# Optimization experiments

Measured on AMD Instinct MI355X. Metric: run time of the kernel, lower is better.

## Reference

```python
import jax, jax.numpy as jnp
import numpy as np

B, N, D = 8, 500, 256
H, W = 480, 640
NUM_CORNERS = 500
MATCH_RADIUS = 1.0
SCORE_RADIUS = 8
BETA = (1.0, 1.0, 1.0)


def _rodrigues(aa):
    theta = jnp.linalg.norm(aa, axis=-1, keepdims=True)
    k = aa / jnp.maximum(theta, 1e-8)
    kx, ky, kz = k[..., 0], k[..., 1], k[..., 2]
    z = jnp.zeros_like(kx)
    Km = jnp.stack([jnp.stack([z, -kz, ky], -1),
                    jnp.stack([kz, z, -kx], -1),
                    jnp.stack([-ky, kx, z], -1)], -2)
    th = theta[..., None]
    return jnp.eye(3) + jnp.sin(th) * Km + (1. - jnp.cos(th)) * (Km @ Km)


def setup_inputs() -> dict:
    key = jax.random.key(0)
    ks = jax.random.split(key, 8)
    descriptors = jax.random.normal(ks[0], (B, N, D), jnp.float32)
    points = jax.random.uniform(ks[1], (B, N, 2), jnp.float32, -1.0, 1.0)
    pointness = jax.random.uniform(ks[2], (B, 1, H, W), jnp.float32) * 0.98 + 0.01
    depths_dense = jax.random.uniform(ks[3], (B, 1, H, W), jnp.float32) * 4.0 + 1.0
    imgs = jax.random.uniform(ks[4], (B, 3, H, W), jnp.float32)
    aa = jax.random.normal(ks[5], (B, 3), jnp.float32) * 0.02
    t = jax.random.normal(ks[6], (B, 3), jnp.float32) * 0.05
    R = _rodrigues(aa)
    poses = jnp.tile(jnp.eye(4, dtype=jnp.float32), (B, 1, 1))
    poses = poses.at[:, :3, :3].set(R).at[:, :3, 3].set(t)
    Kmat = jnp.tile(jnp.array([[300., 0., W / 2.], [0., 300., H / 2.], [0., 0., 1.]], jnp.float32), (B, 1, 1))
    return {"descriptors": descriptors, "points": points, "pointness": pointness,
            "depths_dense": depths_dense, "poses": poses, "K": Kmat, "imgs": imgs}


def denormalize(pts, h, w):
    return jnp.stack([(pts[..., 0] + 1.) * 0.5 * (w - 1), (pts[..., 1] + 1.) * 0.5 * (h - 1)], -1)


def normalize_pix(pts, h, w):
    return jnp.stack([2. * pts[..., 0] / (w - 1) - 1., 2. * pts[..., 1] / (h - 1) - 1.], -1)


def bilinear_sample(img, px):  # img (H,W), px (...,2) pixel coords
    x = jnp.clip(px[..., 0], 0., W - 1.)
    y = jnp.clip(px[..., 1], 0., H - 1.)
    x0 = jnp.floor(x); y0 = jnp.floor(y)
    x1 = jnp.minimum(x0 + 1., W - 1.); y1 = jnp.minimum(y0 + 1., H - 1.)
    wx = x - x0; wy = y - y0
    x0i = x0.astype(jnp.int32); x1i = x1.astype(jnp.int32)
    y0i = y0.astype(jnp.int32); y1i = y1.astype(jnp.int32)
    v00 = img[y0i, x0i]; v01 = img[y0i, x1i]
    v10 = img[y1i, x0i]; v11 = img[y1i, x1i]
    return v00 * (1 - wx) * (1 - wy) + v01 * wx * (1 - wy) + v10 * (1 - wx) * wy + v11 * wx * wy


def pairwise_project(pts, depths, poses, Kmat):
    # pts (B,N,2) normalized; proj[i,j] = points of frame i projected into frame j
    px = denormalize(pts, H, W)
    d = jax.vmap(bilinear_sample)(depths[:, 0], px)  # (B,Np)
    Kinv = jnp.linalg.inv(Kmat)
    homog = jnp.concatenate([px, jnp.ones_like(px[..., :1])], -1)
    Xc = d[..., None] * jnp.einsum('bij,bnj->bni', Kinv, homog)
    Rm = poses[:, :3, :3]; t = poses[:, :3, 3]
    Xw = jnp.einsum('bij,bnj->bni', Rm, Xc) + t[:, None, :]
    diff = Xw[:, None, :, :] - t[None, :, None, :]           # (src,dst,Np,3)
    Xj = jnp.einsum('jba,ijnb->ijna', Rm, diff)              # R_j^T (Xw - t_j)
    uvw = jnp.einsum('jab,ijnb->ijna', Kmat, Xj)
    z = uvw[..., 2]
    zs = jnp.where(jnp.abs(z) < 1e-6, 1e-6, z)
    pn = normalize_pix(jnp.stack([uvw[..., 0] / zs, uvw[..., 1] / zs], -1), H, W)
    invis = (z <= 1e-6) | (jnp.abs(pn[..., 0]) > 1.) | (jnp.abs(pn[..., 1]) > 1.) | (d[:, None, :] <= 0.)
    return pn, invis


def conv2d_same(x, k):
    return jax.lax.conv_general_dilated(x, k[None, None].astype(x.dtype), (1, 1), 'SAME')


_SOBEL_X = np.array([[-1, 0, 1], [-2, 0, 2], [-1, 0, 1]], np.float32) / 8.


def _gauss_kernel(size=7, sigma=1.0):
    r = np.arange(size) - size // 2
    g = np.exp(-r ** 2 / (2 * sigma ** 2)); g /= g.sum()
    return np.outer(g, g).astype(np.float32)


_GAUSS = _gauss_kernel()


def gftt_response(gray):  # min-eigenvalue (Shi-Tomasi) corner response
    gx = conv2d_same(gray, jnp.asarray(_SOBEL_X))
    gy = conv2d_same(gray, jnp.asarray(_SOBEL_X.T))
    g = jnp.asarray(_GAUSS)
    dx2 = conv2d_same(gx * gx, g)
    dy2 = conv2d_same(gy * gy, g)
    dxy = conv2d_same(gx * gy, g)
    tr = dx2 + dy2
    det = dx2 * dy2 - dxy * dxy
    return 0.5 * (tr - jnp.sqrt(jnp.clip(tr * tr - 4. * det, 0.)))


def nms2d(x, k=5):
    mp = jax.lax.reduce_window(x, -jnp.inf, jax.lax.max, (1, 1, k, k), (1, 1, 1, 1), 'SAME')
    return x * (x == mp).astype(x.dtype)


def get_corners(imgs, depths, poses, Kmat):
    gray = (0.299 * imgs[:, 0] + 0.587 * imgs[:, 1] + 0.114 * imgs[:, 2])[:, None]
    c = nms2d(gftt_response(gray))
    r = SCORE_RADIUS
    blocks = c.reshape(B, 1, H // r, r, W // r, r)  # unfold/fold with stride==kernel
    bm = blocks.max(axis=(3, 5), keepdims=True)
    blocks = blocks * ((blocks > 0) & (blocks == bm)).astype(c.dtype)
    c = blocks.reshape(B, 1, H, W)
    vals, idx = jax.lax.top_k(c.reshape(B, -1), NUM_CORNERS)
    xs = (idx % W).astype(jnp.float32)
    ys = (idx // W).astype(jnp.float32)
    coords = normalize_pix(jnp.stack([xs, ys], -1), H, W)
    proj, invis = pairwise_project(coords, depths, poses, Kmat)
    proj = jnp.where(invis[..., None], -2.0, proj)
    combined = jnp.transpose(proj, (1, 0, 2, 3)).reshape(B, B * NUM_CORNERS, 2)  # per dst frame
    pix = jnp.round(denormalize(combined, H, W)).astype(jnp.int32)
    wq, hq = pix[..., 0], pix[..., 1]
    valid = wq >= 0
    v = jnp.tile(vals.reshape(-1), B).reshape(B, B * NUM_CORNERS)
    v = jnp.where(valid, v, 0.)
    hc = jnp.clip(hq, 0, H - 1)
    wc = jnp.clip(wq, 0, W - 1)
    bidx = jnp.broadcast_to(jnp.arange(B)[:, None], (B, B * NUM_CORNERS))
    target = jnp.zeros((B, H, W), imgs.dtype).at[bidx, hc, wc].max(v)
    target = nms2d(target[:, None])
    return (target > 0).astype(imgs.dtype)


def distinction_loss(desc):
    dn = desc / jnp.clip(jnp.linalg.norm(desc, axis=-1, keepdims=True), 1e-8)
    c = jnp.einsum('bnd,bmd->bnm', dn, dn)
    return jax.nn.relu(c).mean()


def match_loss(desc, points, proj, invis):
    p_src = denormalize(jax.lax.stop_gradient(points), H, W)  # (B,N,2)
    p_dst = denormalize(jax.lax.stop_gradient(proj), H, W)    # (src a, dst b, N, 2)
    diff = p_src[None, :, :, None, :] - p_dst[:, :, None, :, :]  # (a,b,n,m,2)
    m = (diff ** 2).sum(-1) <= MATCH_RADIUS ** 2
    m = m & (~invis)[:, :, :, None]                 # zero invisible rows
    n_idx = jnp.arange(N)
    m = m & (n_idx[:, None] < n_idx[None, :])       # triu(diagonal=1)
    dn = desc / jnp.clip(jnp.linalg.norm(desc, axis=-1, keepdims=True), 1e-8)
    cos = jnp.einsum('bnd,amd->abnm', dn, dn)       # cosine(desc[b,n], desc[a,m])
    mf = m.astype(desc.dtype)
    cnt = jnp.maximum(mf.sum(), 1.)
    return ((1. - cos) * mf).sum() / cnt


def bce(p, t):
    logp = jnp.maximum(jnp.log(p), -100.)
    log1p = jnp.maximum(jnp.log(1. - p), -100.)
    return -(t * logp + (1. - t) * log1p).mean()


def reference(descriptors, points, pointness, depths_dense, poses, K, imgs):
    distinction = distinction_loss(descriptors)
    target = get_corners(imgs, depths_dense, poses, K)
    cornerness = bce(pointness, target)
    proj, invis = pairwise_project(points, depths_dense, poses, K)
    match = match_loss(descriptors, points, proj, invis)
    return BETA[0] * distinction + BETA[1] * cornerness + BETA[2] * match
```

## Files before the change

kernel.cpp:

```cpp
#include <hip/hip_runtime.h>
#include <math.h>

#define BB 8
#define NN 500
#define DDIM 256
#define HH 480
#define WW 640
#define HWSZ (HH*WW)
#define BHW (BB*HWSZ)
#define NBLK 4800
#define NOVF 3392
#define NLIST (BB*NN*BB)
#define NBCE2 512
#define NCORR 125
#define NDM 66

#define PD_DIST  0
#define PD_MS    512
#define PD_MC    1024
#define PD_BCE   1536
#define PD_CORR  2560
#define PD_TOTAL 2688

typedef __attribute__((ext_vector_type(8))) short short8;
typedef __attribute__((ext_vector_type(4))) float f32x4;


static __device__ __forceinline__ float wredmaxf(float v) {
  #pragma unroll
  for (int o = 1; o < 64; o <<= 1) v = fmaxf(v, __shfl_xor(v, o, 64));
  return v;
}

static __device__ __forceinline__ double blockRedSum256(double v) {
  __shared__ double sp[4];
  __syncthreads();
  #pragma unroll
  for (int o = 32; o > 0; o >>= 1) v += __shfl_down(v, o, 64);
  int lane = threadIdx.x & 63, wid = threadIdx.x >> 6;
  if (lane == 0) sp[wid] = v;
  __syncthreads();
  double r = 0.0;
  if (threadIdx.x == 0) r = sp[0] + sp[1] + sp[2] + sp[3];
  return r;
}

static __device__ __forceinline__ unsigned short f2bf(float f) {
  unsigned u = __float_as_uint(f);
  return (unsigned short)((u + 0x7FFFu + ((u >> 16) & 1u)) >> 16);
}

static __device__ __forceinline__ float bilin(const float* __restrict__ img, float px, float py) {
  float x = fminf(fmaxf(px, 0.0f), 639.0f);
  float y = fminf(fmaxf(py, 0.0f), 479.0f);
  float x0 = floorf(x), y0 = floorf(y);
  float x1 = fminf(x0 + 1.0f, 639.0f);
  float y1 = fminf(y0 + 1.0f, 479.0f);
  float wx = x - x0, wy = y - y0;
  int x0i = (int)x0, x1i = (int)x1, y0i = (int)y0, y1i = (int)y1;
  float v00 = img[y0i*WW + x0i], v01 = img[y0i*WW + x1i];
  float v10 = img[y1i*WW + x0i], v11 = img[y1i*WW + x1i];
  return v00*(1.0f-wx)*(1.0f-wy) + v01*wx*(1.0f-wy) + v10*(1.0f-wx)*wy + v11*wx*wy;
}

static __device__ void src_compute(float px, float py, const float* __restrict__ dep,
                                   const float* __restrict__ poses, const float* __restrict__ Km,
                                   int bimg, float* Xw, float* dout) {
  float d = bilin(dep, px, py);
  const float* Kb = Km + bimg*9;
  double a00=Kb[0],a01=Kb[1],a02=Kb[2],a10=Kb[3],a11=Kb[4],a12=Kb[5],a20=Kb[6],a21=Kb[7],a22=Kb[8];
  double det = a00*(a11*a22-a12*a21) - a01*(a10*a22-a12*a20) + a02*(a10*a21-a11*a20);
  double id = 1.0/det;
  float i00=(float)((a11*a22-a12*a21)*id), i01=(float)((a02*a21-a01*a22)*id), i02=(float)((a01*a12-a02*a11)*id);
  float i10=(float)((a12*a20-a10*a22)*id), i11=(float)((a00*a22-a02*a20)*id), i12=(float)((a02*a10-a00*a12)*id);
  float i20=(float)((a10*a21-a11*a20)*id), i21=(float)((a01*a20-a00*a21)*id), i22=(float)((a00*a11-a01*a10)*id);
  float c0 = i00*px + i01*py + i02;
  float c1 = i10*px + i11*py + i12;
  float c2 = i20*px + i21*py + i22;
  float X0 = d*c0, X1 = d*c1, X2 = d*c2;
  const float* P = poses + bimg*16;
  Xw[0] = (P[0]*X0 + P[1]*X1 + P[2]*X2)  + P[3];
  Xw[1] = (P[4]*X0 + P[5]*X1 + P[6]*X2)  + P[7];
  Xw[2] = (P[8]*X0 + P[9]*X1 + P[10]*X2) + P[11];
  *dout = d;
}

static __device__ void project_to(const float* __restrict__ poses, const float* __restrict__ Km,
                                  int j, const float* Xw, float dsrc,
                                  float* pnx, float* pny, bool* invis) {
  const float* P = poses + j*16;
  float d0 = Xw[0]-P[3], d1 = Xw[1]-P[7], d2 = Xw[2]-P[11];
  float Xj0 = P[0]*d0 + P[4]*d1 + P[8]*d2;
  float Xj1 = P[1]*d0 + P[5]*d1 + P[9]*d2;
  float Xj2 = P[2]*d0 + P[6]*d1 + P[10]*d2;
  const float* Kb = Km + j*9;
  float u = Kb[0]*Xj0 + Kb[1]*Xj1 + Kb[2]*Xj2;
  float v = Kb[3]*Xj0 + Kb[4]*Xj1 + Kb[5]*Xj2;
  float z = Kb[6]*Xj0 + Kb[7]*Xj1 + Kb[8]*Xj2;
  float zs = (fabsf(z) < 1e-6f) ? 1e-6f : z;
  float pu = u/zs, pv = v/zs;
  float nx = 2.0f*pu/639.0f - 1.0f;
  float ny = 2.0f*pv/479.0f - 1.0f;
  *pnx = nx; *pny = ny;
  *invis = (z <= 1e-6f) || (fabsf(nx) > 1.0f) || (fabsf(ny) > 1.0f) || (dsrc <= 0.0f);
}


__global__ __launch_bounds__(256) void k_front(const float* __restrict__ imgs, float* __restrict__ resp,
                                               int* __restrict__ ovf, int* __restrict__ list,
                                               unsigned int* __restrict__ dnb_u,
                                               const float* __restrict__ desc, float* __restrict__ dn,
                                               unsigned short* __restrict__ dnb,
                                               const float* __restrict__ points, const float* __restrict__ depths,
                                               const float* __restrict__ poses, const float* __restrict__ Km,
                                               float* __restrict__ psrc, float* __restrict__ pdst,
                                               int* __restrict__ minv,
                                               const float* __restrict__ pn, double* __restrict__ pd) {
  __shared__ float smem[6536];
  __shared__ float Gw[7];
  int bid = blockIdx.x, tid = threadIdx.x;
  if (bid < 2400) {
    float* sgxy = smem;
    float* gray = smem + 2888;
    float* hxx  = smem + 2888;
    float* hyy  = hxx + 1216;
    float* hxy  = hyy + 1216;
    int b = bid / 300, r = bid % 300;
    int byi = r / 20, bxi = r % 20;
    int bx = bxi*32, by = byi*32;
    if (bid < 20) {
      int g = bid*256 + tid;
      for (int e = g; e < BB*64; e += 20*256) ovf[e] = 0;
      for (int e = g; e < NLIST; e += 20*256) list[e] = -1;
      for (int e = g; e < 12288; e += 20*256) {
        int bi = e / 1536, rr2 = e % 1536;
        dnb_u[(bi*512 + 500)*128 + rr2] = 0u;
      }
    }
    if (tid < 7) {
      double g[7]; double s = 0.0;
      for (int q = 0; q < 7; q++) { double rr2 = (double)(q-3); g[q] = exp(-(rr2*rr2)/2.0); s += g[q]; }
      Gw[tid] = (float)(g[tid]/s);
    }
    const float* ib = imgs + (size_t)b*3*HWSZ;
    for (int e = tid; e < 40*40; e += 256) {
      int ly = e/40, lx = e%40;
      int X = bx - 4 + lx, Y = by - 4 + ly;
      float v = 0.f;
      if (X>=0 && X<WW && Y>=0 && Y<HH) {
        int p = Y*WW + X;
        v = 0.299f*ib[p] + 0.587f*ib[HWSZ+p] + 0.114f*ib[2*HWSZ+p];
      }
      gray[ly*41+lx] = v;
    }
    __syncthreads();
    const float kxw[3][3] = {{-0.125f,0.f,0.125f},{-0.25f,0.f,0.25f},{-0.125f,0.f,0.125f}};
    for (int e = tid; e < 38*38; e += 256) {
      int rr2 = e/38, c = e%38;
      int X = bx - 3 + c, Y = by - 3 + rr2;
      float sx = 0.f, sy = 0.f;
      #pragma unroll
      for (int i = 0; i < 3; i++)
        #pragma unroll
        for (int j = 0; j < 3; j++) {
          float v = gray[(rr2+i)*41 + (c+j)];
          sx += kxw[i][j]*v;
          sy += kxw[j][i]*v;
        }
      bool in = (X>=0 && X<WW && Y>=0 && Y<HH);
      sgxy[e*2]   = in ? sx : 0.f;
      sgxy[e*2+1] = in ? sy : 0.f;
    }
    __syncthreads();
    for (int e = tid; e < 38*32; e += 256) {
      int rr2 = e >> 5, co = e & 31;
      int base = (rr2*38 + co)*2;
      float axx = 0.f, ayy = 0.f, axy = 0.f;
      #pragma unroll
      for (int j = 0; j < 7; j++) {
        float a = sgxy[base + j*2];
        float c = sgxy[base + j*2 + 1];
        float Gj = Gw[j];
        axx += Gj*(a*a); ayy += Gj*(c*c); axy += Gj*(a*c);
      }
      hxx[e] = axx; hyy[e] = ayy; hxy[e] = axy;
    }
    __syncthreads();
    int tx = tid & 31, ty = tid >> 5;
    int r0 = ty*4;
    float axx[4] = {0,0,0,0}, ayy[4] = {0,0,0,0}, axy[4] = {0,0,0,0};
    #pragma unroll
    for (int rr2 = 0; rr2 < 10; rr2++) {
      int rr3 = r0 + rr2;
      float vxx = hxx[rr3*32+tx], vyy = hyy[rr3*32+tx], vxy = hxy[rr3*32+tx];
      #pragma unroll
      for (int o = 0; o < 4; o++) {
        int i = rr2 - o;
        if (i >= 0 && i <= 6) {
          float Gi = Gw[i];
          axx[o] += Gi*vxx; ayy[o] += Gi*vyy; axy[o] += Gi*vxy;
        }
      }
    }
    #pragma unroll
    for (int o = 0; o < 4; o++) {
      float tr = axx[o] + ayy[o];
      float det = axx[o]*ayy[o] - axy[o]*axy[o];
      float disc = fmaxf(tr*tr - 4.0f*det, 0.f);
      int y = by + r0 + o;
      resp[(size_t)b*HWSZ + y*WW + (bx+tx)] = 0.5f*(tr - sqrtf(disc));
    }
  } else if (bid < 6400) {
    int row = bid - 2400;
    float v = desc[(size_t)row*DDIM + tid];
    float* sp2 = smem;
    float s = v*v;
    #pragma unroll
    for (int o = 32; o > 0; o >>= 1) s += __shfl_down(s, o, 64);
    int lane = tid & 63, wid = tid >> 6;
    if (lane == 0) sp2[wid] = s;
    __syncthreads();
    if (tid == 0) sp2[4] = fmaxf(sqrtf(sp2[0]+sp2[1]+sp2[2]+sp2[3]), 1e-8f);
    __syncthreads();
    float o = v / sp2[4];
    dn[(size_t)row*DDIM + tid] = o;
    int pr = (row/500)*512 + (row%500);
    dnb[(size_t)pr*DDIM + tid] = f2bf(o);
  } else if (bid < 6416) {
    int t = (bid - 6400)*256 + tid;
    if (t < BB*NN) {
      int a = t / NN, m = t % NN;
      float p0 = points[t*2], p1 = points[t*2+1];
      float px = (p0 + 1.0f)*0.5f*639.0f;
      float py = (p1 + 1.0f)*0.5f*479.0f;
      float Xw[3], d;
      src_compute(px, py, depths + (size_t)a*HWSZ, poses, Km, a, Xw, &d);
      psrc[t*2] = px; psrc[t*2+1] = py;
      for (int b = 0; b < BB; b++) {
        float nx, ny; bool inv;
        project_to(poses, Km, b, Xw, d, &nx, &ny, &inv);
        int o = (a*BB + b)*NN + m;
        pdst[o*2]   = (nx + 1.0f)*0.5f*639.0f;
        pdst[o*2+1] = (ny + 1.0f)*0.5f*479.0f;
        minv[o] = inv ? 1 : 0;
      }
    }
  } else {
    int blk = bid - 6416;
    int g = blk*256 + tid;
    double l = 0.0;
    for (int q = g; q < BHW/4; q += NBCE2*256) {
      float4 v = ((const float4*)pn)[q];
      l -= (double)fmaxf(logf(1.f - v.x), -100.f);
      l -= (double)fmaxf(logf(1.f - v.y), -100.f);
      l -= (double)fmaxf(logf(1.f - v.z), -100.f);
      l -= (double)fmaxf(logf(1.f - v.w), -100.f);
    }
    double s = blockRedSum256(l);
    if (tid == 0) pd[PD_BCE + blk] = s;
  }
}

__global__ __launch_bounds__(256) void k_nmscand(const float* __restrict__ resp, float* __restrict__ cv,
                          int* __restrict__ ci, float* __restrict__ cvo,
                          int* __restrict__ cio, int* __restrict__ ovf,
                          float* __restrict__ target) {
  __shared__ float s[36*37];
  __shared__ float hm[36*32];
  __shared__ float c32[32*32];
  int bx = blockIdx.x*32, by = blockIdx.y*32, b = blockIdx.z;
  int tid = threadIdx.x;
  const float* r = resp + (size_t)b*HWSZ;
  for (int e = tid; e < 36*36; e += 256) {
    int ly = e/36, lx = e%36;
    int X = bx - 2 + lx, Y = by - 2 + ly;
    s[ly*37+lx] = (X>=0 && X<WW && Y>=0 && Y<HH) ? r[Y*WW+X] : -INFINITY;
  }
  __syncthreads();
  for (int e = tid; e < 36*32; e += 256) {
    int rr = e >> 5, co = e & 31;
    int base = rr*37 + co;
    float m = s[base];
    m = fmaxf(m, s[base+1]); m = fmaxf(m, s[base+2]);
    m = fmaxf(m, s[base+3]); m = fmaxf(m, s[base+4]);
    hm[e] = m;
  }
  __syncthreads();
  for (int e = tid; e < 1024; e += 256) {
    int y = e >> 5, x = e & 31;
    float mp = hm[y*32+x];
    mp = fmaxf(mp, hm[(y+1)*32+x]); mp = fmaxf(mp, hm[(y+2)*32+x]);
    mp = fmaxf(mp, hm[(y+3)*32+x]); mp = fmaxf(mp, hm[(y+4)*32+x]);
    float v = s[(y+2)*37 + (x+2)];
    c32[e] = (v == mp) ? v : 0.f;
    target[(size_t)b*HWSZ + (by+y)*WW + (bx+x)] = 0.f;
  }
  __syncthreads();
  int wv = tid >> 6, lane = tid & 63;
  int ly8 = lane >> 3, lx8 = lane & 7;
  for (int q = 0; q < 4; q++) {
    int bb = wv*4 + q;
    int oy = (bb >> 2)*8, ox = (bb & 3)*8;
    float cval = c32[(oy+ly8)*32 + ox+lx8];
    float bm = wredmaxf(cval);
    bool win = (cval > 0.f) && (cval == bm);
    unsigned long long mask = __ballot(win);
    int BY = blockIdx.y*4 + (bb >> 2), BX = blockIdx.x*4 + (bb & 3);
    int rblk = BY*80 + BX;
    int gidx = (by+oy+ly8)*WW + (bx+ox+lx8);
    if (mask == 0ull) {
      if (lane == 0) { cv[b*NBLK+rblk] = 0.f; ci[b*NBLK+rblk] = 0; }
    } else if (win) {
      int rank = __popcll(mask & ((1ull << lane) - 1ull));
      if (rank == 0) { cv[b*NBLK+rblk] = cval; ci[b*NBLK+rblk] = gidx; }
      else {
        int pos = atomicAdd(&ovf[b*64], 1);
        if (pos < NOVF) { cvo[b*NOVF+pos] = cval; cio[b*NOVF+pos] = gidx; }
      }
    }
  }
}

__global__ __launch_bounds__(1024) void k_topscat(const float* __restrict__ cv, const int* __restrict__ ci,
                                                  const float* __restrict__ cvo, const int* __restrict__ cio,
                                                  const int* __restrict__ ovf,
                                                  const float* __restrict__ depths, const float* __restrict__ poses,
                                                  const float* __restrict__ Km,
                                                  unsigned int* __restrict__ target, int* __restrict__ list) {
  __shared__ unsigned int hist[16*257];
  __shared__ unsigned int histsum[256];
  __shared__ unsigned long long prefix_s;
  __shared__ int kk_s, fin_s, cgt_s, ceq_s;
  __shared__ float s_topv[NN];
  __shared__ int s_topi[NN];
  int b = blockIdx.x;
  int tid = threadIdx.x;
  int w257 = (tid >> 6)*257;
  int nval = min(ovf[b*64], NOVF);
  unsigned long long kreg[8];
  #pragma unroll
  for (int q = 0; q < 8; q++) {
    int e = tid + q*1024;
    float v = 0.f; unsigned int idx = 0u;
    if (e < NBLK) { v = cv[b*NBLK+e]; idx = (unsigned int)ci[b*NBLK+e]; }
    else if (e - NBLK < nval) { v = cvo[b*NOVF+e-NBLK]; idx = (unsigned int)cio[b*NOVF+e-NBLK]; }
    kreg[q] = ((unsigned long long)__float_as_uint(v) << 32) | (0xFFFFFFFFu - idx);
  }
  if (tid == 0) { prefix_s = 0ull; kk_s = NN; fin_s = -1; cgt_s = 0; ceq_s = 0; }
  for (int e = tid; e < 16*257; e += 1024) hist[e] = 0u;
  __syncthreads();
  for (int round = 0; round < 8; round++) {
    int shift = 56 - 8*round;
    unsigned long long prefix = prefix_s;
    int kk = kk_s;
    unsigned long long himask = (round == 0) ? 0ull : (~0ull << (shift + 8));
    #pragma unroll
    for (int q = 0; q < 8; q++)
      if ((kreg[q] & himask) == prefix)
        atomicAdd(&hist[w257 + (unsigned int)((kreg[q] >> shift) & 255ull)], 1u);
    __syncthreads();
    if (tid < 256) {
      unsigned s = 0u;
      #pragma unroll
      for (int ww = 0; ww < 16; ww++) s += hist[ww*257 + tid];
      histsum[tid] = s;
    }
    __syncthreads();
    for (int e = tid; e < 16*257; e += 1024) hist[e] = 0u;
    if (tid < 64) {
      int l = tid;
      unsigned s0 = histsum[l], s1 = histsum[64+l], s2 = histsum[128+l], s3 = histsum[192+l];
      #pragma unroll
      for (int off = 1; off < 64; off <<= 1) {
        unsigned t0 = __shfl_down(s0, off, 64), t1 = __shfl_down(s1, off, 64);
        unsigned t2 = __shfl_down(s2, off, 64), t3 = __shfl_down(s3, off, 64);
        if (l + off < 64) { s0 += t0; s1 += t1; s2 += t2; s3 += t3; }
      }
      unsigned S1 = __shfl(s1, 0, 64), S2 = __shfl(s2, 0, 64), S3 = __shfl(s3, 0, 64);
      unsigned suf0 = s0 + S1 + S2 + S3, suf1 = s1 + S2 + S3, suf2 = s2 + S3, suf3 = s3;
      int best = -1;
      if      (suf3 >= (unsigned)kk) best = 192 + l;
      else if (suf2 >= (unsigned)kk) best = 128 + l;
      else if (suf1 >= (unsigned)kk) best = 64 + l;
      else if (suf0 >= (unsigned)kk) best = l;
      #pragma unroll
      for (int off = 1; off < 64; off <<= 1) best = max(best, __shfl_xor(best, off, 64));
      if (l == (best & 63)) {
        int seg = best >> 6;
        unsigned sufb = (seg == 3) ? suf3 : ((seg == 2) ? suf2 : ((seg == 1) ? suf1 : suf0));
        unsigned c = histsum[best];
        int Sn = (int)(sufb - c);
        int kkn = kk - Sn;
        prefix_s = prefix | ((unsigned long long)best << shift);
        kk_s = kkn;
        if (kkn == (int)c) fin_s = shift;
      }
    }
    __syncthreads();
    if (fin_s >= 0) break;
  }
  int sg = (fin_s > 0) ? fin_s : 0;
  unsigned long long prefix = prefix_s;
  int kk = kk_s;
  unsigned long long low = (sg > 0) ? ((1ull << sg) - 1ull) : 0ull;
  unsigned long long Tfull = prefix | low;
  unsigned long long mhi = ~low;
  int lane = tid & 63;
  unsigned long long lmask = (1ull << lane) - 1ull;
  #pragma unroll
  for (int q = 0; q < 8; q++) {
    unsigned long long key = kreg[q];
    bool gt = key > Tfull;
    bool eq = !gt && ((key & mhi) == prefix);
    unsigned long long mg = __ballot(gt);
    unsigned long long me = __ballot(eq);
    int slot = -1;
    if (mg != 0ull) {
      int ldr = __ffsll((long long)mg) - 1;
      int baseg = 0;
      if (lane == ldr) baseg = atomicAdd(&cgt_s, (int)__popcll(mg));
      baseg = __shfl(baseg, ldr, 64);
      if (gt) slot = baseg + (int)__popcll(mg & lmask);
    }
    if (me != 0ull) {
      int ldr = __ffsll((long long)me) - 1;
      int basee = 0;
      if (lane == ldr) basee = atomicAdd(&ceq_s, (int)__popcll(me));
      basee = __shfl(basee, ldr, 64);
      if (eq) {
        int p = basee + (int)__popcll(me & lmask);
        if (p < kk) slot = (NN-1) - p;
      }
    }
    if (slot >= 0) {
      s_topv[slot] = __uint_as_float((unsigned int)(key >> 32));
      s_topi[slot] = (int)(0xFFFFFFFFu - (unsigned int)(key & 0xFFFFFFFFull));
    }
  }
  __syncthreads();
  if (tid < NN) {
    float val = s_topv[tid];
    if (val > 0.f) {
      int idx = s_topi[tid];
      float xs = (float)(idx % WW), ys = (float)(idx / WW);
      float cx = 2.0f*xs/639.0f - 1.0f;
      float cy = 2.0f*ys/479.0f - 1.0f;
      float px = (cx + 1.0f)*0.5f*639.0f;
      float py = (cy + 1.0f)*0.5f*479.0f;
      float Xw[3], d;
      src_compute(px, py, depths + (size_t)b*HWSZ, poses, Km, b, Xw, &d);
      int tglob = b*NN + tid;
      for (int j = 0; j < BB; j++) {
        float nx, ny; bool inv;
        project_to(poses, Km, j, Xw, d, &nx, &ny, &inv);
        if (inv) { nx = -2.0f; ny = -2.0f; }
        float fx = rintf((nx + 1.0f)*0.5f*639.0f);
        float fy = rintf((ny + 1.0f)*0.5f*479.0f);
        int wq = (int)fx, hq = (int)fy;
        if (wq < 0) continue;
        int hc = min(max(hq, 0), HH-1), wc = min(max(wq, 0), WW-1);
        int p = j*HWSZ + hc*WW + wc;
        unsigned int old = atomicMax(&target[p], __float_as_uint(val));
        if (old == 0u) list[tglob*BB + j] = p;
      }
    }
  }
}

__global__ __launch_bounds__(256) void k_tail(const float* __restrict__ psrc, const float* __restrict__ pdst,
                                              const int* __restrict__ minv, const float* __restrict__ dn,
                                              const short* __restrict__ dnb,
                                              const int* __restrict__ list, const float* __restrict__ target,
                                              const float* __restrict__ pn, double* __restrict__ pd) {
  __shared__ float sbuf[2500];
  int bid = blockIdx.x, tid = threadIdx.x;
  if (bid < NDM) {
    int w = tid >> 6, lane = tid & 63;
    int gw = bid*4 + w;
    int r16 = lane & 15, koff = (lane >> 4)*8;
    double dsum = 0.0;
    for (int j = 0; j < 16; j++) {
      int jb = gw*16 + j;
      int b = jb / 528, t = jb % 528;
      int I = (int)((sqrtf(8.f*(float)t + 1.f) - 1.f)*0.5f);
      while ((I+1)*(I+2)/2 <= t) I++;
      while (I*(I+1)/2 > t) I--;
      int J = t - I*(I+1)/2;
      const short* bp = dnb + (size_t)b*512*DDIM;
      const short* ap = bp + (I*16 + r16)*DDIM + koff;
      const short* cp = bp + (J*16 + r16)*DDIM + koff;
      f32x4 acc = {0.f, 0.f, 0.f, 0.f};
      #pragma unroll
      for (int kk = 0; kk < 8; kk++) {
        short8 af = *(const short8*)(ap + kk*32);
        short8 bf = *(const short8*)(cp + kk*32);
        acc = __builtin_amdgcn_mfma_f32_16x16x32_bf16(af, bf, acc, 0, 0, 0);
      }
      float ls = fmaxf(acc[0],0.f) + fmaxf(acc[1],0.f) + fmaxf(acc[2],0.f) + fmaxf(acc[3],0.f);
      dsum += (double)ls * ((I == J) ? 1.0 : 2.0);
    }
    double s = blockRedSum256(dsum);
    if (tid == 0) pd[PD_DIST + bid] = s;
  } else if (bid < NDM + 512) {
    int mbid = bid - NDM;
    float* spd = sbuf;
    float* ssrc = sbuf + 1000;
    int* sinv = (int*)(sbuf + 2000);
    int ab = mbid & 63; int b = ab % BB; int a = ab / BB;
    int ys = mbid >> 6;
    for (int e = tid; e < NN; e += 256) {
      spd[e*2]   = pdst[(ab*NN+e)*2];
      spd[e*2+1] = pdst[(ab*NN+e)*2+1];
      sinv[e]    = minv[ab*NN+e];
      ssrc[e*2]   = psrc[(b*NN+e)*2];
      ssrc[e*2+1] = psrc[(b*NN+e)*2+1];
    }
    __syncthreads();
    double lsum = 0.0, lcnt = 0.0;
    for (int mm = ys; mm < NN; mm += 8) {
      float px = spd[mm*2], py = spd[mm*2+1];
      for (int nn = tid; nn < mm; nn += 256) {
        if (sinv[nn]) continue;
        float dx = ssrc[nn*2]   - px;
        float dy = ssrc[nn*2+1] - py;
        if (dx*dx + dy*dy <= 1.0f) {
          const float* da = dn + ((size_t)a*NN + mm)*DDIM;
          const float* db = dn + ((size_t)b*NN + nn)*DDIM;
          float dot = 0.f;
          for (int q = 0; q < DDIM; q++) dot += db[q]*da[q];
          lsum += (double)(1.0f - dot);
          lcnt += 1.0;
        }
      }
    }
    double s = blockRedSum256(lsum);
    if (tid == 0) pd[PD_MS + mbid] = s;
    double c2 = blockRedSum256(lcnt);
    if (tid == 0) pd[PD_MC + mbid] = c2;
  } else {
    int blk = bid - (NDM + 512);
    int g = blk*256 + tid;
    double l = 0.0;
    if (g < NLIST) {
      int p = list[g];
      if (p >= 0) {
        int j = p / HWSZ, pix = p % HWSZ;
        int y = pix / WW, x = pix % WW;
        const float* tb = target + (size_t)j*HWSZ;
        float v = tb[pix];
        float mp = -INFINITY;
        for (int dy = -2; dy <= 2; dy++) {
          int yy = y + dy; if (yy < 0 || yy >= HH) continue;
          for (int dx = -2; dx <= 2; dx++) {
            int xx = x + dx; if (xx < 0 || xx >= WW) continue;
            mp = fmaxf(mp, tb[yy*WW+xx]);
          }
        }
        if (v > 0.f && v == mp) {
          float pv = pn[p];
          l = (double)(-fmaxf(logf(pv), -100.f)) + (double)fmaxf(logf(1.f - pv), -100.f);
        }
      }
    }
    double s = blockRedSum256(l);
    if (tid == 0) pd[PD_CORR + blk] = s;
  }
}

__global__ void k_final(const double* __restrict__ pd, float* __restrict__ out) {
  int tid = threadIdx.x;
  double l;
  l = 0.0; for (int i = tid; i < NDM;   i += 256) l += pd[PD_DIST + i];
  double dist = blockRedSum256(l);
  l = 0.0; for (int i = tid; i < 512;   i += 256) l += pd[PD_MS + i];
  double ms = blockRedSum256(l);
  l = 0.0; for (int i = tid; i < 512;   i += 256) l += pd[PD_MC + i];
  double mc = blockRedSum256(l);
  l = 0.0; for (int i = tid; i < NBCE2; i += 256) l += pd[PD_BCE + i];
  double bce = blockRedSum256(l);
  l = 0.0; for (int i = tid; i < NCORR; i += 256) l += pd[PD_CORR + i];
  double corr = blockRedSum256(l);
  if (tid == 0) {
    float distf = (float)(dist / (double)(BB*NN*NN));
    float cornf = (float)((bce + corr) / (double)BHW);
    float cntf  = fmaxf((float)mc, 1.0f);
    float matchf = (float)ms / cntf;
    out[0] = distf + cornf + matchf;
  }
}


extern "C" void kernel_launch(void* const* d_in, const int* in_sizes, int n_in,
                              void* d_out, int out_size, void* d_ws, size_t ws_size,
                              hipStream_t stream) {
  (void)in_sizes; (void)n_in; (void)out_size; (void)ws_size;
  const float* desc      = (const float*)d_in[0];
  const float* points    = (const float*)d_in[1];
  const float* pointness = (const float*)d_in[2];
  const float* depths    = (const float*)d_in[3];
  const float* poses     = (const float*)d_in[4];
  const float* Kmat      = (const float*)d_in[5];
  const float* imgs      = (const float*)d_in[6];
  float* out = (float*)d_out;

  double* pd = (double*)d_ws;
  float* f = (float*)(pd + PD_TOTAL);
  float* bufA = f;
  float* bufC = bufA + (size_t)BHW;
  float* cv_main = bufC + (size_t)BHW;
  int*   ci_main = (int*)(cv_main + BB*NBLK);
  float* cv_ovf  = (float*)(ci_main + BB*NBLK);
  int*   ci_ovf  = (int*)(cv_ovf + BB*NOVF);
  int*   ovf     = (int*)(ci_ovf + BB*NOVF);
  float* psrc = (float*)(ovf + BB*64);
  float* pdst = psrc + BB*NN*2;
  int*   minv = (int*)(pdst + BB*BB*NN*2);
  float* dn   = (float*)(minv + BB*BB*NN);
  int*   list = (int*)(dn + (size_t)BB*NN*DDIM);
  unsigned short* dnb = (unsigned short*)(list + NLIST);

  dim3 tgrid(WW/32, HH/32, BB);

  k_front  <<<6928, 256, 0, stream>>>(imgs, bufA, ovf, list, (unsigned int*)dnb,
                                      desc, dn, dnb, points, depths, poses, Kmat,
                                      psrc, pdst, minv, pointness, pd);
  k_nmscand<<<tgrid, 256, 0, stream>>>(bufA, cv_main, ci_main, cv_ovf, ci_ovf, ovf, bufC);
  k_topscat<<<BB, 1024, 0, stream>>>(cv_main, ci_main, cv_ovf, ci_ovf, ovf,
                                     depths, poses, Kmat, (unsigned int*)bufC, list);
  k_tail   <<<NDM + 512 + NCORR, 256, 0, stream>>>(psrc, pdst, minv, dn, (const short*)dnb,
                                                   list, bufC, pointness, pd);
  k_final  <<<1, 256, 0, stream>>>(pd, out);
}
```

Measured before the change: 110.4 us.

## Merge descriptor and match losses into NMS kernel and fuse final reduction

```diff
diff --git a/kernel.cpp b/kernel.cpp
--- a/kernel.cpp
+++ b/kernel.cpp
@@ -108,7 +108,7 @@
 
 __global__ __launch_bounds__(256) void k_front(const float* __restrict__ imgs, float* __restrict__ resp,
                                                int* __restrict__ ovf, int* __restrict__ list,
-                                               unsigned int* __restrict__ dnb_u,
+                                               unsigned int* __restrict__ dnb_u, int* __restrict__ done,
                                                const float* __restrict__ desc, float* __restrict__ dn,
                                                unsigned short* __restrict__ dnb,
                                                const float* __restrict__ points, const float* __restrict__ depths,
@@ -130,6 +130,7 @@
     int bx = bxi*32, by = byi*32;
     if (bid < 20) {
       int g = bid*256 + tid;
+      if (g == 0) *done = 0;
       for (int e = g; e < BB*64; e += 20*256) ovf[e] = 0;
       for (int e = g; e < NLIST; e += 20*256) list[e] = -1;
       for (int e = g; e < 12288; e += 20*256) {
@@ -261,61 +262,133 @@
   }
 }
 
-__global__ __launch_bounds__(256) void k_nmscand(const float* __restrict__ resp, float* __restrict__ cv,
-                          int* __restrict__ ci, float* __restrict__ cvo,
-                          int* __restrict__ cio, int* __restrict__ ovf,
-                          float* __restrict__ target) {
-  __shared__ float s[36*37];
-  __shared__ float hm[36*32];
-  __shared__ float c32[32*32];
-  int bx = blockIdx.x*32, by = blockIdx.y*32, b = blockIdx.z;
-  int tid = threadIdx.x;
-  const float* r = resp + (size_t)b*HWSZ;
-  for (int e = tid; e < 36*36; e += 256) {
-    int ly = e/36, lx = e%36;
-    int X = bx - 2 + lx, Y = by - 2 + ly;
-    s[ly*37+lx] = (X>=0 && X<WW && Y>=0 && Y<HH) ? r[Y*WW+X] : -INFINITY;
-  }
-  __syncthreads();
-  for (int e = tid; e < 36*32; e += 256) {
-    int rr = e >> 5, co = e & 31;
-    int base = rr*37 + co;
-    float m = s[base];
-    m = fmaxf(m, s[base+1]); m = fmaxf(m, s[base+2]);
-    m = fmaxf(m, s[base+3]); m = fmaxf(m, s[base+4]);
-    hm[e] = m;
-  }
-  __syncthreads();
-  for (int e = tid; e < 1024; e += 256) {
-    int y = e >> 5, x = e & 31;
-    float mp = hm[y*32+x];
-    mp = fmaxf(mp, hm[(y+1)*32+x]); mp = fmaxf(mp, hm[(y+2)*32+x]);
-    mp = fmaxf(mp, hm[(y+3)*32+x]); mp = fmaxf(mp, hm[(y+4)*32+x]);
-    float v = s[(y+2)*37 + (x+2)];
-    c32[e] = (v == mp) ? v : 0.f;
-    target[(size_t)b*HWSZ + (by+y)*WW + (bx+x)] = 0.f;
-  }
-  __syncthreads();
-  int wv = tid >> 6, lane = tid & 63;
-  int ly8 = lane >> 3, lx8 = lane & 7;
-  for (int q = 0; q < 4; q++) {
-    int bb = wv*4 + q;
-    int oy = (bb >> 2)*8, ox = (bb & 3)*8;
-    float cval = c32[(oy+ly8)*32 + ox+lx8];
-    float bm = wredmaxf(cval);
-    bool win = (cval > 0.f) && (cval == bm);
-    unsigned long long mask = __ballot(win);
-    int BY = blockIdx.y*4 + (bb >> 2), BX = blockIdx.x*4 + (bb & 3);
-    int rblk = BY*80 + BX;
-    int gidx = (by+oy+ly8)*WW + (bx+ox+lx8);
-    if (mask == 0ull) {
-      if (lane == 0) { cv[b*NBLK+rblk] = 0.f; ci[b*NBLK+rblk] = 0; }
-    } else if (win) {
-      int rank = __popcll(mask & ((1ull << lane) - 1ull));
-      if (rank == 0) { cv[b*NBLK+rblk] = cval; ci[b*NBLK+rblk] = gidx; }
-      else {
-        int pos = atomicAdd(&ovf[b*64], 1);
-        if (pos < NOVF) { cvo[b*NOVF+pos] = cval; cio[b*NOVF+pos] = gidx; }
+__global__ __launch_bounds__(256) void k_mid(const float* __restrict__ resp, float* __restrict__ cv,
+                                             int* __restrict__ ci, float* __restrict__ cvo,
+                                             int* __restrict__ cio, int* __restrict__ ovf,
+                                             float* __restrict__ target,
+                                             const float* __restrict__ psrc, const float* __restrict__ pdst,
+                                             const int* __restrict__ minv, const float* __restrict__ dn,
+                                             const short* __restrict__ dnb, double* __restrict__ pd) {
+  __shared__ float sbuf[3508];
+  int bid = blockIdx.x, tid = threadIdx.x;
+  if (bid < NDM) {
+    int w = tid >> 6, lane = tid & 63;
+    int gw = bid*4 + w;
+    int r16 = lane & 15, koff = (lane >> 4)*8;
+    double dsum = 0.0;
+    for (int j = 0; j < 16; j++) {
+      int jb = gw*16 + j;
+      int b = jb / 528, t = jb % 528;
+      int I = (int)((sqrtf(8.f*(float)t + 1.f) - 1.f)*0.5f);
+      while ((I+1)*(I+2)/2 <= t) I++;
+      while (I*(I+1)/2 > t) I--;
+      int J = t - I*(I+1)/2;
+      const short* bp = dnb + (size_t)b*512*DDIM;
+      const short* ap = bp + (I*16 + r16)*DDIM + koff;
+      const short* cp = bp + (J*16 + r16)*DDIM + koff;
+      f32x4 acc = {0.f, 0.f, 0.f, 0.f};
+      #pragma unroll
+      for (int kk = 0; kk < 8; kk++) {
+        short8 af = *(const short8*)(ap + kk*32);
+        short8 bf = *(const short8*)(cp + kk*32);
+        acc = __builtin_amdgcn_mfma_f32_16x16x32_bf16(af, bf, acc, 0, 0, 0);
+      }
+      float ls = fmaxf(acc[0],0.f) + fmaxf(acc[1],0.f) + fmaxf(acc[2],0.f) + fmaxf(acc[3],0.f);
+      dsum += (double)ls * ((I == J) ? 1.0 : 2.0);
+    }
+    double s = blockRedSum256(dsum);
+    if (tid == 0) pd[PD_DIST + bid] = s;
+  } else if (bid < NDM + 512) {
+    int mbid = bid - NDM;
+    float* spd = sbuf;
+    float* ssrc = sbuf + 1000;
+    int* sinv = (int*)(sbuf + 2000);
+    int ab = mbid & 63; int b = ab % BB; int a = ab / BB;
+    int ys = mbid >> 6;
+    for (int e = tid; e < NN; e += 256) {
+      spd[e*2]   = pdst[(ab*NN+e)*2];
+      spd[e*2+1] = pdst[(ab*NN+e)*2+1];
+      sinv[e]    = minv[ab*NN+e];
+      ssrc[e*2]   = psrc[(b*NN+e)*2];
+      ssrc[e*2+1] = psrc[(b*NN+e)*2+1];
+    }
+    __syncthreads();
+    double lsum = 0.0, lcnt = 0.0;
+    for (int mm = ys; mm < NN; mm += 8) {
+      float px = spd[mm*2], py = spd[mm*2+1];
+      for (int nn = tid; nn < mm; nn += 256) {
+        if (sinv[nn]) continue;
+        float dx = ssrc[nn*2]   - px;
+        float dy = ssrc[nn*2+1] - py;
+        if (dx*dx + dy*dy <= 1.0f) {
+          const float* da = dn + ((size_t)a*NN + mm)*DDIM;
+          const float* db = dn + ((size_t)b*NN + nn)*DDIM;
+          float dot = 0.f;
+          for (int q = 0; q < DDIM; q++) dot += db[q]*da[q];
+          lsum += (double)(1.0f - dot);
+          lcnt += 1.0;
+        }
+      }
+    }
+    double s = blockRedSum256(lsum);
+    if (tid == 0) pd[PD_MS + mbid] = s;
+    double c2 = blockRedSum256(lcnt);
+    if (tid == 0) pd[PD_MC + mbid] = c2;
+  } else {
+    int nb = bid - (NDM + 512);
+    int b = nb / 300, r = nb % 300;
+    int byi = r / 20, bxi = r % 20;
+    int bx = bxi*32, by = byi*32;
+    float* s = sbuf;
+    float* hm = sbuf + 1332;
+    float* c32 = sbuf + 2484;
+    const float* rp = resp + (size_t)b*HWSZ;
+    for (int e = tid; e < 36*36; e += 256) {
+      int ly = e/36, lx = e%36;
+      int X = bx - 2 + lx, Y = by - 2 + ly;
+      s[ly*37+lx] = (X>=0 && X<WW && Y>=0 && Y<HH) ? rp[Y*WW+X] : -INFINITY;
+    }
+    __syncthreads();
+    for (int e = tid; e < 36*32; e += 256) {
+      int rr = e >> 5, co = e & 31;
+      int base = rr*37 + co;
+      float m = s[base];
+      m = fmaxf(m, s[base+1]); m = fmaxf(m, s[base+2]);
+      m = fmaxf(m, s[base+3]); m = fmaxf(m, s[base+4]);
+      hm[e] = m;
+    }
+    __syncthreads();
+    for (int e = tid; e < 1024; e += 256) {
+      int y = e >> 5, x = e & 31;
+      float mp = hm[y*32+x];
+      mp = fmaxf(mp, hm[(y+1)*32+x]); mp = fmaxf(mp, hm[(y+2)*32+x]);
+      mp = fmaxf(mp, hm[(y+3)*32+x]); mp = fmaxf(mp, hm[(y+4)*32+x]);
+      float v = s[(y+2)*37 + (x+2)];
+      c32[e] = (v == mp) ? v : 0.f;
+      target[(size_t)b*HWSZ + (by+y)*WW + (bx+x)] = 0.f;
+    }
+    __syncthreads();
+    int wv = tid >> 6, lane = tid & 63;
+    int ly8 = lane >> 3, lx8 = lane & 7;
+    for (int q = 0; q < 4; q++) {
+      int bb = wv*4 + q;
+      int oy = (bb >> 2)*8, ox = (bb & 3)*8;
+      float cval = c32[(oy+ly8)*32 + ox+lx8];
+      float bm = wredmaxf(cval);
+      bool win = (cval > 0.f) && (cval == bm);
+      unsigned long long mask = __ballot(win);
+      int BY = byi*4 + (bb >> 2), BX = bxi*4 + (bb & 3);
+      int rblk = BY*80 + BX;
+      int gidx = (by+oy+ly8)*WW + (bx+ox+lx8);
+      if (mask == 0ull) {
+        if (lane == 0) { cv[b*NBLK+rblk] = 0.f; ci[b*NBLK+rblk] = 0; }
+      } else if (win) {
+        int rank = __popcll(mask & ((1ull << lane) - 1ull));
+        if (rank == 0) { cv[b*NBLK+rblk] = cval; ci[b*NBLK+rblk] = gidx; }
+        else {
+          int pos = atomicAdd(&ovf[b*64], 1);
+          if (pos < NOVF) { cvo[b*NOVF+pos] = cval; cio[b*NOVF+pos] = gidx; }
+        }
       }
     }
   }
@@ -467,125 +540,62 @@
   }
 }
 
-__global__ __launch_bounds__(256) void k_tail(const float* __restrict__ psrc, const float* __restrict__ pdst,
-                                              const int* __restrict__ minv, const float* __restrict__ dn,
-                                              const short* __restrict__ dnb,
-                                              const int* __restrict__ list, const float* __restrict__ target,
-                                              const float* __restrict__ pn, double* __restrict__ pd) {
-  __shared__ float sbuf[2500];
-  int bid = blockIdx.x, tid = threadIdx.x;
-  if (bid < NDM) {
-    int w = tid >> 6, lane = tid & 63;
-    int gw = bid*4 + w;
-    int r16 = lane & 15, koff = (lane >> 4)*8;
-    double dsum = 0.0;
-    for (int j = 0; j < 16; j++) {
-      int jb = gw*16 + j;
-      int b = jb / 528, t = jb % 528;
-      int I = (int)((sqrtf(8.f*(float)t + 1.f) - 1.f)*0.5f);
-      while ((I+1)*(I+2)/2 <= t) I++;
-      while (I*(I+1)/2 > t) I--;
-      int J = t - I*(I+1)/2;
-      const short* bp = dnb + (size_t)b*512*DDIM;
-      const short* ap = bp + (I*16 + r16)*DDIM + koff;
-      const short* cp = bp + (J*16 + r16)*DDIM + koff;
-      f32x4 acc = {0.f, 0.f, 0.f, 0.f};
-      #pragma unroll
-      for (int kk = 0; kk < 8; kk++) {
-        short8 af = *(const short8*)(ap + kk*32);
-        short8 bf = *(const short8*)(cp + kk*32);
-        acc = __builtin_amdgcn_mfma_f32_16x16x32_bf16(af, bf, acc, 0, 0, 0);
-      }
-      float ls = fmaxf(acc[0],0.f) + fmaxf(acc[1],0.f) + fmaxf(acc[2],0.f) + fmaxf(acc[3],0.f);
-      dsum += (double)ls * ((I == J) ? 1.0 : 2.0);
-    }
-    double s = blockRedSum256(dsum);
-    if (tid == 0) pd[PD_DIST + bid] = s;
-  } else if (bid < NDM + 512) {
-    int mbid = bid - NDM;
-    float* spd = sbuf;
-    float* ssrc = sbuf + 1000;
-    int* sinv = (int*)(sbuf + 2000);
-    int ab = mbid & 63; int b = ab % BB; int a = ab / BB;
-    int ys = mbid >> 6;
-    for (int e = tid; e < NN; e += 256) {
-      spd[e*2]   = pdst[(ab*NN+e)*2];
-      spd[e*2+1] = pdst[(ab*NN+e)*2+1];
-      sinv[e]    = minv[ab*NN+e];
-      ssrc[e*2]   = psrc[(b*NN+e)*2];
-      ssrc[e*2+1] = psrc[(b*NN+e)*2+1];
-    }
-    __syncthreads();
-    double lsum = 0.0, lcnt = 0.0;
-    for (int mm = ys; mm < NN; mm += 8) {
-      float px = spd[mm*2], py = spd[mm*2+1];
-      for (int nn = tid; nn < mm; nn += 256) {
-        if (sinv[nn]) continue;
-        float dx = ssrc[nn*2]   - px;
-        float dy = ssrc[nn*2+1] - py;
-        if (dx*dx + dy*dy <= 1.0f) {
-          const float* da = dn + ((size_t)a*NN + mm)*DDIM;
-          const float* db = dn + ((size_t)b*NN + nn)*DDIM;
-          float dot = 0.f;
-          for (int q = 0; q < DDIM; q++) dot += db[q]*da[q];
-          lsum += (double)(1.0f - dot);
-          lcnt += 1.0;
+__global__ __launch_bounds__(256) void k_last(const int* __restrict__ list, const float* __restrict__ target,
+                                              const float* __restrict__ pn, double* __restrict__ pd,
+                                              int* __restrict__ done, float* __restrict__ out) {
+  __shared__ int lastf;
+  int blk = blockIdx.x, tid = threadIdx.x;
+  int g = blk*256 + tid;
+  double l = 0.0;
+  if (g < NLIST) {
+    int p = list[g];
+    if (p >= 0) {
+      int j = p / HWSZ, pix = p % HWSZ;
+      int y = pix / WW, x = pix % WW;
+      const float* tb = target + (size_t)j*HWSZ;
+      float v = tb[pix];
+      float mp = -INFINITY;
+      for (int dy = -2; dy <= 2; dy++) {
+        int yy = y + dy; if (yy < 0 || yy >= HH) continue;
+        for (int dx = -2; dx <= 2; dx++) {
+          int xx = x + dx; if (xx < 0 || xx >= WW) continue;
+          mp = fmaxf(mp, tb[yy*WW+xx]);
         }
       }
-    }
-    double s = blockRedSum256(lsum);
-    if (tid == 0) pd[PD_MS + mbid] = s;
-    double c2 = blockRedSum256(lcnt);
-    if (tid == 0) pd[PD_MC + mbid] = c2;
-  } else {
-    int blk = bid - (NDM + 512);
-    int g = blk*256 + tid;
-    double l = 0.0;
-    if (g < NLIST) {
-      int p = list[g];
-      if (p >= 0) {
-        int j = p / HWSZ, pix = p % HWSZ;
-        int y = pix / WW, x = pix % WW;
-        const float* tb = target + (size_t)j*HWSZ;
-        float v = tb[pix];
-        float mp = -INFINITY;
-        for (int dy = -2; dy <= 2; dy++) {
-          int yy = y + dy; if (yy < 0 || yy >= HH) continue;
-          for (int dx = -2; dx <= 2; dx++) {
-            int xx = x + dx; if (xx < 0 || xx >= WW) continue;
-            mp = fmaxf(mp, tb[yy*WW+xx]);
-          }
-        }
-        if (v > 0.f && v == mp) {
-          float pv = pn[p];
-          l = (double)(-fmaxf(logf(pv), -100.f)) + (double)fmaxf(logf(1.f - pv), -100.f);
-        }
-      }
-    }
-    double s = blockRedSum256(l);
-    if (tid == 0) pd[PD_CORR + blk] = s;
-  }
-}
-
-__global__ void k_final(const double* __restrict__ pd, float* __restrict__ out) {
-  int tid = threadIdx.x;
-  double l;
-  l = 0.0; for (int i = tid; i < NDM;   i += 256) l += pd[PD_DIST + i];
-  double dist = blockRedSum256(l);
-  l = 0.0; for (int i = tid; i < 512;   i += 256) l += pd[PD_MS + i];
-  double ms = blockRedSum256(l);
-  l = 0.0; for (int i = tid; i < 512;   i += 256) l += pd[PD_MC + i];
-  double mc = blockRedSum256(l);
-  l = 0.0; for (int i = tid; i < NBCE2; i += 256) l += pd[PD_BCE + i];
-  double bce = blockRedSum256(l);
-  l = 0.0; for (int i = tid; i < NCORR; i += 256) l += pd[PD_CORR + i];
-  double corr = blockRedSum256(l);
+      if (v > 0.f && v == mp) {
+        float pv = pn[p];
+        l = (double)(-fmaxf(logf(pv), -100.f)) + (double)fmaxf(logf(1.f - pv), -100.f);
+      }
+    }
+  }
+  double s = blockRedSum256(l);
   if (tid == 0) {
-    float distf = (float)(dist / (double)(BB*NN*NN));
-    float cornf = (float)((bce + corr) / (double)BHW);
-    float cntf  = fmaxf((float)mc, 1.0f);
-    float matchf = (float)ms / cntf;
-    out[0] = distf + cornf + matchf;
+    pd[PD_CORR + blk] = s;
+    __threadfence();
+    int t = atomicAdd(done, 1);
+    lastf = (t == NCORR - 1) ? 1 : 0;
+  }
+  __syncthreads();
+  if (lastf) {
+    __threadfence();
+    double l2;
+    l2 = 0.0; for (int i = tid; i < NDM;   i += 256) l2 += pd[PD_DIST + i];
+    double dist = blockRedSum256(l2);
+    l2 = 0.0; for (int i = tid; i < 512;   i += 256) l2 += pd[PD_MS + i];
+    double ms = blockRedSum256(l2);
+    l2 = 0.0; for (int i = tid; i < 512;   i += 256) l2 += pd[PD_MC + i];
+    double mc = blockRedSum256(l2);
+    l2 = 0.0; for (int i = tid; i < NBCE2; i += 256) l2 += pd[PD_BCE + i];
+    double bce = blockRedSum256(l2);
+    l2 = 0.0; for (int i = tid; i < NCORR; i += 256) l2 += pd[PD_CORR + i];
+    double corr = blockRedSum256(l2);
+    if (tid == 0) {
+      float distf = (float)(dist / (double)(BB*NN*NN));
+      float cornf = (float)((bce + corr) / (double)BHW);
+      float cntf  = fmaxf((float)mc, 1.0f);
+      float matchf = (float)ms / cntf;
+      out[0] = distf + cornf + matchf;
+    }
   }
 }
 
@@ -618,16 +628,14 @@
   float* dn   = (float*)(minv + BB*BB*NN);
   int*   list = (int*)(dn + (size_t)BB*NN*DDIM);
   unsigned short* dnb = (unsigned short*)(list + NLIST);
-
-  dim3 tgrid(WW/32, HH/32, BB);
-
-  k_front  <<<6928, 256, 0, stream>>>(imgs, bufA, ovf, list, (unsigned int*)dnb,
+  int*   done = (int*)(dnb + (size_t)BB*512*DDIM);
+
+  k_front  <<<6928, 256, 0, stream>>>(imgs, bufA, ovf, list, (unsigned int*)dnb, done,
                                       desc, dn, dnb, points, depths, poses, Kmat,
                                       psrc, pdst, minv, pointness, pd);
-  k_nmscand<<<tgrid, 256, 0, stream>>>(bufA, cv_main, ci_main, cv_ovf, ci_ovf, ovf, bufC);
+  k_mid    <<<NDM + 512 + 2400, 256, 0, stream>>>(bufA, cv_main, ci_main, cv_ovf, ci_ovf, ovf, bufC,
+                                                  psrc, pdst, minv, dn, (const short*)dnb, pd);
   k_topscat<<<BB, 1024, 0, stream>>>(cv_main, ci_main, cv_ovf, ci_ovf, ovf,
                                      depths, poses, Kmat, (unsigned int*)bufC, list);
-  k_tail   <<<NDM + 512 + NCORR, 256, 0, stream>>>(psrc, pdst, minv, dn, (const short*)dnb,
-                                                   list, bufC, pointness, pd);
-  k_final  <<<1, 256, 0, stream>>>(pd, out);
-}
+  k_last   <<<NCORR, 256, 0, stream>>>(list, bufC, pointness, pd, done, out);
+}
```

After: 110.5 us. Within noise of the previous version (+0.0%).
